# Kernel tuning notes

Hardware: AMD Instinct MI355X
Metric: run time of the kernel (lower is better)

Reference implementation:

```python
import jax, jax.numpy as jnp
import numpy as np

NUM_SUBSPACES = 8
CODEBOOK_SIZE = 256
SUBSPACE_DIM = 96


def setup_inputs() -> dict:
    key = jax.random.key(0)
    k1, k2 = jax.random.split(key)
    embeddings = jax.random.normal(k1, (16, 4096, NUM_SUBSPACES * SUBSPACE_DIM), dtype=jnp.float32)
    codebooks = jax.random.normal(k2, (NUM_SUBSPACES, CODEBOOK_SIZE, SUBSPACE_DIM), dtype=jnp.float32)
    return {"embeddings": embeddings, "codebooks": codebooks}


def reference(embeddings, codebooks):
    # embeddings: [B, S, E] with E = M*d; codebooks: [M, K, d]
    B, S, E = embeddings.shape
    M, K, d = codebooks.shape
    # [N, M, d] -> [M, N, d] so each subspace is contiguous
    x = embeddings.reshape(B * S, M, d).transpose(1, 0, 2)
    x2 = jnp.sum(x * x, axis=-1, keepdims=True)              # [M, N, 1]
    c2 = jnp.sum(codebooks * codebooks, axis=-1)[:, None, :]  # [M, 1, K]
    xc = jnp.einsum('mnd,mkd->mnk', x, codebooks)             # [M, N, K]
    dist2 = x2 - 2.0 * xc + c2                                # [M, N, K]
    # argmin over codes (same result as cdist p=2 argmin since sqrt is monotone)
    idx = jnp.argmin(dist2, axis=-1)                          # [M, N]
    # gather nearest codewords per subspace
    quantized = codebooks[jnp.arange(M)[:, None], idx]        # [M, N, d]
    # reassemble: [N, M, d] -> [B, S, E]
    return quantized.transpose(1, 0, 2).reshape(B, S, E)
```

## Files before the change

### kernel.cpp

```cpp
#include <hip/hip_runtime.h>

typedef _Float16 h8 __attribute__((ext_vector_type(8)));
typedef unsigned short u16x8 __attribute__((ext_vector_type(8)));
typedef float   f32x16 __attribute__((ext_vector_type(16)));

constexpr int NSUB  = 8;
constexpr int NCODE = 256;
constexpr int SDIM  = 96;
constexpr int EMB   = NSUB * SDIM;
constexpr float C_SHIFT = 192.0f;
constexpr float THR = 0.04f;

constexpr size_t WS_FRAG_BYTES = (size_t)NSUB * 3072 * 16;
constexpr size_t WS_NEEDED     = WS_FRAG_BYTES + (size_t)NSUB * NCODE * 4;

__device__ __forceinline__ unsigned short f2bf(float v) {
    unsigned u = __builtin_bit_cast(unsigned, v);
    u = u + 0x7FFFu + ((u >> 16) & 1u);
    return (unsigned short)(u >> 16);
}

__global__ __launch_bounds__(256) void pq_prep_h(const float* __restrict__ cb,
                                                 unsigned short* __restrict__ wsf,
                                                 float* __restrict__ wsc2)
{
    const int m   = (int)blockIdx.x;
    const int tid = (int)threadIdx.x;
    {
        const float* c = cb + ((size_t)m * NCODE + tid) * SDIM;
        double s = 0.0;
        for (int k = 0; k < SDIM; ++k) { double v = (double)c[k]; s += v * v; }
        wsc2[m * NCODE + tid] = (float)(0.5 * s + (double)C_SHIFT);
    }
    for (int i = 0; i < 12; ++i) {
        int idx = i * 256 + tid;
        int l   = idx & 63;
        int u   = idx >> 6;
        int s   = u % 6;
        int t   = u / 6;
        int code = t * 32 + (l & 31);
        int k0   = s * 16 + (l >> 5) * 8;
        const float* src = cb + (size_t)m * NCODE * SDIM + (size_t)code * SDIM + k0;
        u16x8 o;
        #pragma unroll
        for (int j = 0; j < 8; ++j) {
            _Float16 hv = (_Float16)(-src[j]);
            o[j] = __builtin_bit_cast(unsigned short, hv);
        }
        *(u16x8*)(wsf + ((size_t)m * 3072 + idx) * 8) = o;
    }
}

__global__ __launch_bounds__(128) void pq_mfma17(
    const float* __restrict__ emb,
    const float* __restrict__ cb,
    const unsigned short* __restrict__ wsf,
    const float* __restrict__ wsc2,
    float* __restrict__ out,
    int nrows,
    int rowblks)
{
    const int tid  = (int)threadIdx.x;
    const int lane = tid & 63;
    const int hib  = lane >> 5;
    const int m    = (int)blockIdx.x & 7;
    const int rb   = ((int)blockIdx.x >> 3) * 2 + (tid >> 6);
    if (rb >= rowblks) return;
    const int row0 = rb * 32;

    const unsigned short* wb = wsf + (size_t)m * 3072 * 8;
    const float* c2p = wsc2 + m * NCODE;

    h8 xh[6];
    {
        int r = row0 + (lane & 31);
        if (r >= nrows) r = nrows - 1;
        const float* xr = emb + (size_t)r * EMB + m * SDIM + hib * 8;
        #pragma unroll
        for (int s = 0; s < 6; ++s) {
            float4 v0 = *(const float4*)(xr + s * 16);
            float4 v1 = *(const float4*)(xr + s * 16 + 4);
            float v[8] = { v0.x, v0.y, v0.z, v0.w, v1.x, v1.y, v1.z, v1.w };
            #pragma unroll
            for (int j = 0; j < 8; ++j) xh[s][j] = (_Float16)v[j];
        }
    }

    float b1 = 3.4e38f, b2 = 3.4e38f, b3 = 3.4e38f;
    int   i1 = 1 << 30,  i2 = 1 << 30,  i3 = 1 << 30;
    #pragma unroll 1
    for (int p = 0; p < 4; ++p) {
        const int t0 = p * 2, t1 = t0 + 1;
        f32x16 a0, a1;
        #pragma unroll
        for (int rq = 0; rq < 4; ++rq) {
            float4 q0 = *(const float4*)(c2p + t0 * 32 + rq * 8 + hib * 4);
            float4 q1 = *(const float4*)(c2p + t1 * 32 + rq * 8 + hib * 4);
            a0[rq*4+0]=q0.x; a0[rq*4+1]=q0.y; a0[rq*4+2]=q0.z; a0[rq*4+3]=q0.w;
            a1[rq*4+0]=q1.x; a1[rq*4+1]=q1.y; a1[rq*4+2]=q1.z; a1[rq*4+3]=q1.w;
        }
        __builtin_amdgcn_s_setprio(1);
        #pragma unroll
        for (int s = 0; s < 6; ++s) {
            h8 c0 = *(const h8*)(wb + (size_t)((t0 * 6 + s) * 64 + lane) * 8);
            h8 c1 = *(const h8*)(wb + (size_t)((t1 * 6 + s) * 64 + lane) * 8);
            a0 = __builtin_amdgcn_mfma_f32_32x32x16_f16(c0, xh[s], a0, 0, 0, 0);
            a1 = __builtin_amdgcn_mfma_f32_32x32x16_f16(c1, xh[s], a1, 0, 0, 0);
        }
        __builtin_amdgcn_s_setprio(0);
        #pragma unroll
        for (int r = 0; r < 16; ++r) {
            float sv = a0[r];
            int   kv = t0 * 32 + (r & 3) + 8 * (r >> 2) + hib * 4;
            if (sv < b1)      { b3 = b2; i3 = i2; b2 = b1; i2 = i1; b1 = sv; i1 = kv; }
            else if (sv < b2) { b3 = b2; i3 = i2; b2 = sv; i2 = kv; }
            else if (sv < b3) { b3 = sv; i3 = kv; }
        }
        #pragma unroll
        for (int r = 0; r < 16; ++r) {
            float sv = a1[r];
            int   kv = t1 * 32 + (r & 3) + 8 * (r >> 2) + hib * 4;
            if (sv < b1)      { b3 = b2; i3 = i2; b2 = b1; i2 = i1; b1 = sv; i1 = kv; }
            else if (sv < b2) { b3 = b2; i3 = i2; b2 = sv; i2 = kv; }
            else if (sv < b3) { b3 = sv; i3 = kv; }
        }
    }
    {
        float ob1 = __shfl_xor(b1, 32), ob2 = __shfl_xor(b2, 32), ob3 = __shfl_xor(b3, 32);
        int   oi1 = __shfl_xor(i1, 32), oi2 = __shfl_xor(i2, 32), oi3 = __shfl_xor(i3, 32);
        auto ins = [&](float s, int i) {
            if (s < b1 || (s == b1 && i < i1))      { b3 = b2; i3 = i2; b2 = b1; i2 = i1; b1 = s; i1 = i; }
            else if (s < b2 || (s == b2 && i < i2)) { b3 = b2; i3 = i2; b2 = s; i2 = i; }
            else if (s < b3 || (s == b3 && i < i3)) { b3 = s; i3 = i; }
        };
        ins(ob1, oi1); ins(ob2, oi2); ins(ob3, oi3);
    }

    {
        int grow = row0 + (lane & 31);
        if (lane < 32 && grow < nrows && (b2 - b1 < THR)) {
            int i3e = (b3 - b1 < THR) ? i3 : i1;
            const float* xr = emb + (size_t)grow * EMB + m * SDIM;
            const float* p1 = cb + ((size_t)m * NCODE + i1)  * SDIM;
            const float* p2 = cb + ((size_t)m * NCODE + i2)  * SDIM;
            const float* p3 = cb + ((size_t)m * NCODE + i3e) * SDIM;
            double d1 = 0.0, d2 = 0.0, d3 = 0.0;
            for (int kk = 0; kk < SDIM; ++kk) {
                double xv = (double)xr[kk];
                double e1 = xv - (double)p1[kk];
                double e2 = xv - (double)p2[kk];
                double e3 = xv - (double)p3[kk];
                d1 += e1 * e1; d2 += e2 * e2; d3 += e3 * e3;
            }
            double bd = d1; int bi = i1;
            if (d2 < bd || (d2 == bd && i2  < bi)) { bd = d2; bi = i2; }
            if (d3 < bd || (d3 == bd && i3e < bi)) { bd = d3; bi = i3e; }
            i1 = bi;
        }
    }

    #pragma unroll
    for (int ii = 0; ii < 12; ++ii) {
        int Q = ii * 64 + lane;
        int r = Q / 24, f = Q % 24;
        int grow = row0 + r;
        int k = __shfl(i1, r);
        if (grow < nrows) {
            float4 v = *(const float4*)(cb + ((size_t)m * NCODE + k) * SDIM + f * 4);
            *(float4*)(out + (size_t)grow * EMB + m * SDIM + f * 4) = v;
        }
    }
}

__global__ __launch_bounds__(256) void pq_argmin_kernel(
    const float* __restrict__ emb, const float* __restrict__ cb,
    float* __restrict__ out, int nrows)
{
    const int m   = (int)(blockIdx.x & 7);
    const int row = (int)(blockIdx.x >> 3) * 256 + (int)threadIdx.x;
    const float* __restrict__ cbm = cb + (size_t)m * (NCODE * SDIM);
    __shared__ float half_c2[NCODE];
    {
        const int k = (int)threadIdx.x;
        const float* c = cbm + k * SDIM;
        float s = 0.f;
        #pragma unroll
        for (int i = 0; i < SDIM; i += 4) {
            const float4 v = *reinterpret_cast<const float4*>(c + i);
            s = fmaf(v.x, v.x, s); s = fmaf(v.y, v.y, s);
            s = fmaf(v.z, v.z, s); s = fmaf(v.w, v.w, s);
        }
        half_c2[k] = 0.5f * s;
    }
    __syncthreads();
    if (row >= nrows) return;
    float x[SDIM];
    {
        const float* xr = emb + (size_t)row * EMB + m * SDIM;
        #pragma unroll
        for (int i = 0; i < SDIM; i += 4) {
            const float4 v = *reinterpret_cast<const float4*>(xr + i);
            x[i+0] = v.x; x[i+1] = v.y; x[i+2] = v.z; x[i+3] = v.w;
        }
    }
    float best = 3.4e38f, best2 = 3.4e38f;
    int bestk = 0, bestk2 = 0;
    #pragma unroll 1
    for (int k = 0; k < NCODE; k += 4) {
        const float* c0 = cbm + (k + 0) * SDIM;
        const float* c1 = cbm + (k + 1) * SDIM;
        const float* c2 = cbm + (k + 2) * SDIM;
        const float* c3 = cbm + (k + 3) * SDIM;
        float a0 = 0.f, a1 = 0.f, a2 = 0.f, a3 = 0.f;
        #pragma unroll
        for (int i = 0; i < SDIM; i += 4) {
            const float4 v0 = *reinterpret_cast<const float4*>(c0 + i);
            const float4 v1 = *reinterpret_cast<const float4*>(c1 + i);
            const float4 v2 = *reinterpret_cast<const float4*>(c2 + i);
            const float4 v3 = *reinterpret_cast<const float4*>(c3 + i);
            a0 = fmaf(x[i+0], v0.x, a0); a0 = fmaf(x[i+1], v0.y, a0);
            a0 = fmaf(x[i+2], v0.z, a0); a0 = fmaf(x[i+3], v0.w, a0);
            a1 = fmaf(x[i+0], v1.x, a1); a1 = fmaf(x[i+1], v1.y, a1);
            a1 = fmaf(x[i+2], v1.z, a1); a1 = fmaf(x[i+3], v1.w, a1);
            a2 = fmaf(x[i+0], v2.x, a2); a2 = fmaf(x[i+1], v2.y, a2);
            a2 = fmaf(x[i+2], v2.z, a2); a2 = fmaf(x[i+3], v2.w, a2);
            a3 = fmaf(x[i+0], v3.x, a3); a3 = fmaf(x[i+1], v3.y, a3);
            a3 = fmaf(x[i+2], v3.z, a3); a3 = fmaf(x[i+3], v3.w, a3);
        }
        const float s[4] = { half_c2[k+0] - a0, half_c2[k+1] - a1,
                             half_c2[k+2] - a2, half_c2[k+3] - a3 };
        #pragma unroll
        for (int j = 0; j < 4; ++j) {
            if (s[j] < best)       { best2 = best; bestk2 = bestk; best = s[j]; bestk = k + j; }
            else if (s[j] < best2) { best2 = s[j]; bestk2 = k + j; }
        }
    }
    if (best2 - best < 0.02f) {
        const float* ca = cbm + bestk  * SDIM;
        const float* cbv = cbm + bestk2 * SDIM;
        double da = 0.0, db = 0.0;
        for (int i = 0; i < SDIM; ++i) {
            const double ea = (double)x[i] - (double)ca[i];
            const double eb = (double)x[i] - (double)cbv[i];
            da += ea * ea; db += eb * eb;
        }
        if (db < da || (db == da && bestk2 < bestk)) bestk = bestk2;
    }
    const float* cbest = cbm + bestk * SDIM;
    float* o = out + (size_t)row * EMB + m * SDIM;
    #pragma unroll
    for (int i = 0; i < SDIM; i += 4)
        *reinterpret_cast<float4*>(o + i) = *reinterpret_cast<const float4*>(cbest + i);
}

extern "C" void kernel_launch(void* const* d_in, const int* in_sizes, int n_in,
                              void* d_out, int out_size, void* d_ws, size_t ws_size,
                              hipStream_t stream) {
    const float* emb = (const float*)d_in[0];
    const float* cb  = (const float*)d_in[1];
    float* out = (float*)d_out;
    const int nrows = in_sizes[0] / EMB;

    if (ws_size < WS_NEEDED) {
        const int rowBlocks = (nrows + 255) / 256;
        pq_argmin_kernel<<<dim3(rowBlocks * NSUB), dim3(256), 0, stream>>>(emb, cb, out, nrows);
        return;
    }

    unsigned short* wsf = (unsigned short*)d_ws;
    float* wsc2 = (float*)((char*)d_ws + WS_FRAG_BYTES);

    pq_prep_h<<<dim3(NSUB), dim3(256), 0, stream>>>(cb, wsf, wsc2);

    const int rowblks = (nrows + 31) / 32;
    const int nb      = ((rowblks + 1) / 2) * NSUB;
    pq_mfma17<<<dim3(nb), dim3(128), 0, stream>>>(emb, cb, wsf, wsc2, out, nrows, rowblks);
}
```

Before: 194.5 us.

## Defer ambiguous-row repair to a separate exhaustive fp64 kernel via global worklist

```diff
diff --git a/kernel.cpp b/kernel.cpp
--- a/kernel.cpp
+++ b/kernel.cpp
@@ -12,13 +12,10 @@
 constexpr float THR = 0.04f;
 
 constexpr size_t WS_FRAG_BYTES = (size_t)NSUB * 3072 * 16;
-constexpr size_t WS_NEEDED     = WS_FRAG_BYTES + (size_t)NSUB * NCODE * 4;
-
-__device__ __forceinline__ unsigned short f2bf(float v) {
-    unsigned u = __builtin_bit_cast(unsigned, v);
-    u = u + 0x7FFFu + ((u >> 16) & 1u);
-    return (unsigned short)(u >> 16);
-}
+constexpr size_t C2_BYTES      = (size_t)NSUB * NCODE * 4;
+constexpr size_t CNT_OFF       = WS_FRAG_BYTES + C2_BYTES;
+constexpr size_t LIST_OFF      = CNT_OFF + 16;
+constexpr size_t WS_NEEDED     = LIST_OFF + 65536 * 4;
 
 __global__ __launch_bounds__(256) void pq_prep_h(const float* __restrict__ cb,
                                                  unsigned short* __restrict__ wsf,
@@ -51,12 +48,15 @@
     }
 }
 
-__global__ __launch_bounds__(128) void pq_mfma17(
+__global__ __launch_bounds__(128) void pq_mfma20(
     const float* __restrict__ emb,
     const float* __restrict__ cb,
     const unsigned short* __restrict__ wsf,
     const float* __restrict__ wsc2,
     float* __restrict__ out,
+    unsigned* __restrict__ gcnt,
+    unsigned* __restrict__ glist,
+    unsigned cap,
     int nrows,
     int rowblks)
 {
@@ -86,8 +86,8 @@
         }
     }
 
-    float b1 = 3.4e38f, b2 = 3.4e38f, b3 = 3.4e38f;
-    int   i1 = 1 << 30,  i2 = 1 << 30,  i3 = 1 << 30;
+    float b1 = 3.4e38f, b2 = 3.4e38f;
+    int   i1 = 1 << 30;
     #pragma unroll 1
     for (int p = 0; p < 4; ++p) {
         const int t0 = p * 2, t1 = t0 + 1;
@@ -112,50 +112,32 @@
         for (int r = 0; r < 16; ++r) {
             float sv = a0[r];
             int   kv = t0 * 32 + (r & 3) + 8 * (r >> 2) + hib * 4;
-            if (sv < b1)      { b3 = b2; i3 = i2; b2 = b1; i2 = i1; b1 = sv; i1 = kv; }
-            else if (sv < b2) { b3 = b2; i3 = i2; b2 = sv; i2 = kv; }
-            else if (sv < b3) { b3 = sv; i3 = kv; }
+            if (sv < b1)      { b2 = b1; b1 = sv; i1 = kv; }
+            else if (sv < b2) { b2 = sv; }
         }
         #pragma unroll
         for (int r = 0; r < 16; ++r) {
             float sv = a1[r];
             int   kv = t1 * 32 + (r & 3) + 8 * (r >> 2) + hib * 4;
-            if (sv < b1)      { b3 = b2; i3 = i2; b2 = b1; i2 = i1; b1 = sv; i1 = kv; }
-            else if (sv < b2) { b3 = b2; i3 = i2; b2 = sv; i2 = kv; }
-            else if (sv < b3) { b3 = sv; i3 = kv; }
-        }
-    }
-    {
-        float ob1 = __shfl_xor(b1, 32), ob2 = __shfl_xor(b2, 32), ob3 = __shfl_xor(b3, 32);
-        int   oi1 = __shfl_xor(i1, 32), oi2 = __shfl_xor(i2, 32), oi3 = __shfl_xor(i3, 32);
-        auto ins = [&](float s, int i) {
-            if (s < b1 || (s == b1 && i < i1))      { b3 = b2; i3 = i2; b2 = b1; i2 = i1; b1 = s; i1 = i; }
-            else if (s < b2 || (s == b2 && i < i2)) { b3 = b2; i3 = i2; b2 = s; i2 = i; }
-            else if (s < b3 || (s == b3 && i < i3)) { b3 = s; i3 = i; }
-        };
-        ins(ob1, oi1); ins(ob2, oi2); ins(ob3, oi3);
+            if (sv < b1)      { b2 = b1; b1 = sv; i1 = kv; }
+            else if (sv < b2) { b2 = sv; }
+        }
+    }
+    {
+        float ob1 = __shfl_xor(b1, 32);
+        int   oi1 = __shfl_xor(i1, 32);
+        float ob2 = __shfl_xor(b2, 32);
+        bool o_better = (ob1 < b1) || (ob1 == b1 && oi1 < i1);
+        float loser = o_better ? b1 : ob1;
+        if (o_better) { b1 = ob1; i1 = oi1; }
+        b2 = fminf(fminf(b2, ob2), loser);
     }
 
     {
         int grow = row0 + (lane & 31);
         if (lane < 32 && grow < nrows && (b2 - b1 < THR)) {
-            int i3e = (b3 - b1 < THR) ? i3 : i1;
-            const float* xr = emb + (size_t)grow * EMB + m * SDIM;
-            const float* p1 = cb + ((size_t)m * NCODE + i1)  * SDIM;
-            const float* p2 = cb + ((size_t)m * NCODE + i2)  * SDIM;
-            const float* p3 = cb + ((size_t)m * NCODE + i3e) * SDIM;
-            double d1 = 0.0, d2 = 0.0, d3 = 0.0;
-            for (int kk = 0; kk < SDIM; ++kk) {
-                double xv = (double)xr[kk];
-                double e1 = xv - (double)p1[kk];
-                double e2 = xv - (double)p2[kk];
-                double e3 = xv - (double)p3[kk];
-                d1 += e1 * e1; d2 += e2 * e2; d3 += e3 * e3;
-            }
-            double bd = d1; int bi = i1;
-            if (d2 < bd || (d2 == bd && i2  < bi)) { bd = d2; bi = i2; }
-            if (d3 < bd || (d3 == bd && i3e < bi)) { bd = d3; bi = i3e; }
-            i1 = bi;
+            unsigned pos = atomicAdd(gcnt, 1u);
+            if (pos < cap) glist[pos] = (unsigned)grow | ((unsigned)m << 20);
         }
     }
 
@@ -168,6 +150,54 @@
         if (grow < nrows) {
             float4 v = *(const float4*)(cb + ((size_t)m * NCODE + k) * SDIM + f * 4);
             *(float4*)(out + (size_t)grow * EMB + m * SDIM + f * 4) = v;
+        }
+    }
+}
+
+__global__ __launch_bounds__(256) void pq_repair(
+    const float* __restrict__ emb,
+    const float* __restrict__ cb,
+    float* __restrict__ out,
+    const unsigned* __restrict__ gcnt,
+    const unsigned* __restrict__ glist,
+    unsigned cap)
+{
+    const int tid  = (int)threadIdx.x;
+    const int lane = tid & 63;
+    const unsigned wv = (unsigned)blockIdx.x * 4u + (unsigned)(tid >> 6);
+    unsigned n = *gcnt; if (n > cap) n = cap;
+    for (unsigned j = wv; j < n; j += 4096u) {
+        unsigned e = glist[j];
+        int grow = (int)(e & 0xFFFFFu);
+        int m    = (int)(e >> 20);
+        const float* xr = emb + (size_t)grow * EMB + m * SDIM;
+        double bd = 1e300; int bc = NCODE;
+        #pragma unroll 1
+        for (int qc = 0; qc < 4; ++qc) {
+            int code = qc * 64 + lane;
+            const float* cv = cb + ((size_t)m * NCODE + code) * SDIM;
+            double acc = 0.0;
+            #pragma unroll
+            for (int kk = 0; kk < SDIM; kk += 4) {
+                float4 xv = *(const float4*)(xr + kk);
+                float4 cc = *(const float4*)(cv + kk);
+                double d0 = (double)xv.x - (double)cc.x;
+                double d1 = (double)xv.y - (double)cc.y;
+                double d2 = (double)xv.z - (double)cc.z;
+                double d3 = (double)xv.w - (double)cc.w;
+                acc += d0*d0 + d1*d1 + d2*d2 + d3*d3;
+            }
+            if (acc < bd) { bd = acc; bc = code; }
+        }
+        #pragma unroll
+        for (int off = 32; off > 0; off >>= 1) {
+            double od = __shfl_xor(bd, off);
+            int    oc = __shfl_xor(bc, off);
+            if (od < bd || (od == bd && oc < bc)) { bd = od; bc = oc; }
+        }
+        if (lane < 24) {
+            float4 v = *(const float4*)(cb + ((size_t)m * NCODE + bc) * SDIM + lane * 4);
+            *(float4*)(out + (size_t)grow * EMB + m * SDIM + lane * 4) = v;
         }
     }
 }
@@ -268,11 +298,17 @@
     }
 
     unsigned short* wsf = (unsigned short*)d_ws;
-    float* wsc2 = (float*)((char*)d_ws + WS_FRAG_BYTES);
-
+    float*    wsc2  = (float*)((char*)d_ws + WS_FRAG_BYTES);
+    unsigned* gcnt  = (unsigned*)((char*)d_ws + CNT_OFF);
+    unsigned* glist = (unsigned*)((char*)d_ws + LIST_OFF);
+    unsigned  cap   = (unsigned)((ws_size - LIST_OFF) / 4);
+
+    hipMemsetAsync(gcnt, 0, 4, stream);
     pq_prep_h<<<dim3(NSUB), dim3(256), 0, stream>>>(cb, wsf, wsc2);
 
     const int rowblks = (nrows + 31) / 32;
     const int nb      = ((rowblks + 1) / 2) * NSUB;
-    pq_mfma17<<<dim3(nb), dim3(128), 0, stream>>>(emb, cb, wsf, wsc2, out, nrows, rowblks);
-}
+    pq_mfma20<<<dim3(nb), dim3(128), 0, stream>>>(emb, cb, wsf, wsc2, out,
+                                                  gcnt, glist, cap, nrows, rowblks);
+    pq_repair<<<dim3(1024), dim3(256), 0, stream>>>(emb, cb, out, gcnt, glist, cap);
+}
```

New measurement: 228.4 us. 1.17x slower.

## Defer ambiguous-argmin double-precision repair to a separate wave-parallel kernel

Applied to the files above, without the earlier changes.

```diff
diff --git a/kernel.cpp b/kernel.cpp
--- a/kernel.cpp
+++ b/kernel.cpp
@@ -12,13 +12,10 @@
 constexpr float THR = 0.04f;
 
 constexpr size_t WS_FRAG_BYTES = (size_t)NSUB * 3072 * 16;
-constexpr size_t WS_NEEDED     = WS_FRAG_BYTES + (size_t)NSUB * NCODE * 4;
-
-__device__ __forceinline__ unsigned short f2bf(float v) {
-    unsigned u = __builtin_bit_cast(unsigned, v);
-    u = u + 0x7FFFu + ((u >> 16) & 1u);
-    return (unsigned short)(u >> 16);
-}
+constexpr size_t C2_BYTES      = (size_t)NSUB * NCODE * 4;
+constexpr size_t CNT_OFF       = WS_FRAG_BYTES + C2_BYTES;
+constexpr size_t LIST_OFF      = CNT_OFF + 16;
+constexpr size_t WS_NEEDED     = LIST_OFF + 49000 * 8;
 
 __global__ __launch_bounds__(256) void pq_prep_h(const float* __restrict__ cb,
                                                  unsigned short* __restrict__ wsf,
@@ -51,12 +48,15 @@
     }
 }
 
-__global__ __launch_bounds__(128) void pq_mfma17(
+__global__ __launch_bounds__(128) void pq_mfma22(
     const float* __restrict__ emb,
     const float* __restrict__ cb,
     const unsigned short* __restrict__ wsf,
     const float* __restrict__ wsc2,
     float* __restrict__ out,
+    unsigned* __restrict__ gcnt,
+    uint2* __restrict__ glist,
+    unsigned cap,
     int nrows,
     int rowblks)
 {
@@ -140,22 +140,10 @@
         int grow = row0 + (lane & 31);
         if (lane < 32 && grow < nrows && (b2 - b1 < THR)) {
             int i3e = (b3 - b1 < THR) ? i3 : i1;
-            const float* xr = emb + (size_t)grow * EMB + m * SDIM;
-            const float* p1 = cb + ((size_t)m * NCODE + i1)  * SDIM;
-            const float* p2 = cb + ((size_t)m * NCODE + i2)  * SDIM;
-            const float* p3 = cb + ((size_t)m * NCODE + i3e) * SDIM;
-            double d1 = 0.0, d2 = 0.0, d3 = 0.0;
-            for (int kk = 0; kk < SDIM; ++kk) {
-                double xv = (double)xr[kk];
-                double e1 = xv - (double)p1[kk];
-                double e2 = xv - (double)p2[kk];
-                double e3 = xv - (double)p3[kk];
-                d1 += e1 * e1; d2 += e2 * e2; d3 += e3 * e3;
-            }
-            double bd = d1; int bi = i1;
-            if (d2 < bd || (d2 == bd && i2  < bi)) { bd = d2; bi = i2; }
-            if (d3 < bd || (d3 == bd && i3e < bi)) { bd = d3; bi = i3e; }
-            i1 = bi;
+            unsigned pos = atomicAdd(gcnt, 1u);
+            if (pos < cap)
+                glist[pos] = make_uint2((unsigned)grow | ((unsigned)m << 20),
+                                        (unsigned)i1 | ((unsigned)i2 << 8) | ((unsigned)i3e << 16));
         }
     }
 
@@ -168,6 +156,63 @@
         if (grow < nrows) {
             float4 v = *(const float4*)(cb + ((size_t)m * NCODE + k) * SDIM + f * 4);
             *(float4*)(out + (size_t)grow * EMB + m * SDIM + f * 4) = v;
+        }
+    }
+}
+
+__global__ __launch_bounds__(256) void pq_repair3(
+    const float* __restrict__ emb,
+    const float* __restrict__ cb,
+    float* __restrict__ out,
+    const unsigned* __restrict__ gcnt,
+    const uint2* __restrict__ glist,
+    unsigned cap)
+{
+    const int tid  = (int)threadIdx.x;
+    const int lane = tid & 63;
+    const bool act = lane < 24;
+    const int  dof = act ? lane * 4 : 0;
+    const unsigned wv = (unsigned)blockIdx.x * 4u + (unsigned)(tid >> 6);
+    unsigned n = *gcnt; if (n > cap) n = cap;
+
+    for (unsigned j = wv; j < n; j += 4096u) {
+        uint2 e = glist[j];
+        int grow = (int)(e.x & 0xFFFFFu);
+        int m    = (int)(e.x >> 20);
+        int c1   = (int)(e.y & 0xFFu);
+        int c2   = (int)((e.y >> 8) & 0xFFu);
+        int c3   = (int)((e.y >> 16) & 0xFFu);
+        const float* xr  = emb + (size_t)grow * EMB + m * SDIM;
+        const float* cbm = cb + (size_t)m * NCODE * SDIM;
+
+        float4 xv = act ? *(const float4*)(xr + dof) : make_float4(0.f, 0.f, 0.f, 0.f);
+
+        auto dist = [&](int code) -> double {
+            double par = 0.0;
+            if (act) {
+                float4 cc = *(const float4*)(cbm + (size_t)code * SDIM + dof);
+                double d0 = (double)xv.x - (double)cc.x;
+                double d1 = (double)xv.y - (double)cc.y;
+                double d2 = (double)xv.z - (double)cc.z;
+                double d3 = (double)xv.w - (double)cc.w;
+                par = d0*d0 + d1*d1 + d2*d2 + d3*d3;
+            }
+            #pragma unroll
+            for (int off = 32; off > 0; off >>= 1)
+                par += __shfl_xor(par, off);
+            return par;
+        };
+        double d1 = dist(c1);
+        double d2 = dist(c2);
+        double d3 = dist(c3);
+
+        int bi = c1; double bd = d1;
+        if (d2 < bd || (d2 == bd && c2 < bi)) { bd = d2; bi = c2; }
+        if (d3 < bd || (d3 == bd && c3 < bi)) { bd = d3; bi = c3; }
+
+        if (act) {
+            float4 v = *(const float4*)(cbm + (size_t)bi * SDIM + dof);
+            *(float4*)(out + (size_t)grow * EMB + m * SDIM + dof) = v;
         }
     }
 }
@@ -268,11 +313,17 @@
     }
 
     unsigned short* wsf = (unsigned short*)d_ws;
-    float* wsc2 = (float*)((char*)d_ws + WS_FRAG_BYTES);
-
+    float*    wsc2  = (float*)((char*)d_ws + WS_FRAG_BYTES);
+    unsigned* gcnt  = (unsigned*)((char*)d_ws + CNT_OFF);
+    uint2*    glist = (uint2*)((char*)d_ws + LIST_OFF);
+    unsigned  cap   = (unsigned)((ws_size - LIST_OFF) / 8);
+
+    hipMemsetAsync(gcnt, 0, 4, stream);
     pq_prep_h<<<dim3(NSUB), dim3(256), 0, stream>>>(cb, wsf, wsc2);
 
     const int rowblks = (nrows + 31) / 32;
     const int nb      = ((rowblks + 1) / 2) * NSUB;
-    pq_mfma17<<<dim3(nb), dim3(128), 0, stream>>>(emb, cb, wsf, wsc2, out, nrows, rowblks);
-}
+    pq_mfma22<<<dim3(nb), dim3(128), 0, stream>>>(emb, cb, wsf, wsc2, out,
+                                                  gcnt, glist, cap, nrows, rowblks);
+    pq_repair3<<<dim3(1024), dim3(256), 0, stream>>>(emb, cb, out, gcnt, glist, cap);
+}
```

Result: no change. 197.6 us (+1.6%).
